# Kernel optimization log

Hardware: AMD Instinct MI355X
Metric: run time of the kernel (lower is better)

## Reference

```python
import jax, jax.numpy as jnp
import numpy as np

N_NODES = 100000

def setup_inputs() -> dict:
    key = jax.random.key(0)
    k1, k2, k3, k4 = jax.random.split(key, 4)
    feat = jax.random.normal(k1, (N_NODES, 128), dtype=jnp.float32)
    weight = jax.random.normal(k2, (128, 64), dtype=jnp.float32) * 0.05
    src = jax.random.randint(k3, (600000,), 0, N_NODES, dtype=jnp.int64)
    dst = jax.random.randint(k4, (600000,), 0, N_NODES, dtype=jnp.int64)
    return {"feat": feat, "weight": weight, "src": src, "dst": dst}

def reference(feat, weight, src, dst):
    n = feat.shape[0]
    ones = jnp.ones(src.shape[0], dtype=jnp.float32)
    # out-degree of source nodes (edges leave src), in-degree of dst nodes
    out_deg = jnp.clip(jax.ops.segment_sum(ones, src, num_segments=n), 1.0)
    in_deg = jnp.clip(jax.ops.segment_sum(ones, dst, num_segments=n), 1.0)
    norm_src = (out_deg ** -0.5)[:, None]   # [N,1]
    norm_dst = (in_deg ** -0.5)[:, None]    # [N,1]
    # in_feats (128) > out_feats (64): project first, then aggregate
    h = jnp.matmul(feat, weight) * norm_src              # [N, 64]
    msgs = h[src]                                        # [E, 64] gather
    rst = jax.ops.segment_sum(msgs, dst, num_segments=n)  # [N, 64] scatter-sum
    rst = rst * norm_dst
    return rst
```

## Files before the change

### kernel.cpp

```cpp
#include <hip/hip_runtime.h>
#include <hip/hip_fp16.h>

#define IN_F 128
#define OUT_F 64
#define NB    256
#define BSH   9
#define CAP   3840
#define CHUNK 2048
#define KPF  136
#define KPW  144

using short8  = __attribute__((ext_vector_type(8))) short;
using float4v = __attribute__((ext_vector_type(4))) float;

static __device__ inline unsigned short f2bf(float x) {
    union { float f; unsigned u; } v; v.f = x;
    unsigned r = (v.u + 0x7fffu + ((v.u >> 16) & 1u)) >> 16;
    return (unsigned short)r;
}

__global__ __launch_bounds__(256) void bin_gemm_kernel(
    const int* __restrict__ src, const int* __restrict__ dst,
    int* __restrict__ gcur_d, int* __restrict__ gcur_s,
    unsigned* __restrict__ bkt_d, unsigned short* __restrict__ bkt_s,
    int E, int nbin,
    const float* __restrict__ feat, const float* __restrict__ W,
    __half* __restrict__ h, int n)
{
    __shared__ union {
        struct { int hd[NB]; int hs[NB]; int based[NB]; int bases[NB]; } bin;
        struct { unsigned short Fh[128 * KPF]; unsigned short Wt[64 * KPW]; } gm;
    } smem;

    const int tid = threadIdx.x;

    if (blockIdx.x < (unsigned)nbin) {
        const int e0 = blockIdx.x * CHUNK;

        smem.bin.hd[tid] = 0; smem.bin.hs[tid] = 0;
        __syncthreads();

        int sv[8], dv[8];
        #pragma unroll
        for (int j = 0; j < 8; ++j) {
            int i = e0 + j * 256 + tid;
            if (i < E) { sv[j] = src[i]; dv[j] = dst[i]; }
            else       { sv[j] = -1;     dv[j] = -1; }
        }
        #pragma unroll
        for (int j = 0; j < 8; ++j) {
            if (dv[j] >= 0) {
                atomicAdd(&smem.bin.hd[dv[j] >> BSH], 1);
                atomicAdd(&smem.bin.hs[sv[j] >> BSH], 1);
            }
        }
        __syncthreads();

        int cd = smem.bin.hd[tid], cs = smem.bin.hs[tid];
        smem.bin.based[tid] = cd ? atomicAdd(&gcur_d[tid], cd) : 0;
        smem.bin.bases[tid] = cs ? atomicAdd(&gcur_s[tid], cs) : 0;
        smem.bin.hd[tid] = 0; smem.bin.hs[tid] = 0;
        __syncthreads();

        #pragma unroll
        for (int j = 0; j < 8; ++j) {
            if (dv[j] >= 0) {
                int bd = dv[j] >> BSH;
                int pd = atomicAdd(&smem.bin.hd[bd], 1) + smem.bin.based[bd];
                if (pd < CAP)
                    bkt_d[(size_t)bd * CAP + pd] =
                        (unsigned)sv[j] | ((unsigned)(dv[j] & 511) << 17);
                int bs = sv[j] >> BSH;
                int ps = atomicAdd(&smem.bin.hs[bs], 1) + smem.bin.bases[bs];
                if (ps < CAP) bkt_s[(size_t)bs * CAP + ps] = (unsigned short)(sv[j] & 511);
            }
        }
        return;
    }

    unsigned short* Fh = smem.gm.Fh;
    unsigned short* Wt = smem.gm.Wt;
    const int row0 = (blockIdx.x - nbin) * 128;

    {
        const float4* W4 = (const float4*)W;
        #pragma unroll
        for (int it = 0; it < 8; ++it) {
            int i4 = it * 256 + tid;
            int k  = i4 >> 4;
            int c4 = (i4 & 15) * 4;
            float4 wv = W4[i4];
            Wt[(c4 + 0) * KPW + k] = f2bf(wv.x);
            Wt[(c4 + 1) * KPW + k] = f2bf(wv.y);
            Wt[(c4 + 2) * KPW + k] = f2bf(wv.z);
            Wt[(c4 + 3) * KPW + k] = f2bf(wv.w);
        }
    }
    {
        const float4* F4 = (const float4*)feat;
        #pragma unroll
        for (int it = 0; it < 16; ++it) {
            int i4 = it * 256 + tid;
            int r  = i4 >> 5;
            int c4 = (i4 & 31) * 4;
            int gr = row0 + r; if (gr >= n) gr = n - 1;
            float4 v = F4[(long)gr * 32 + (i4 & 31)];
            ushort4 u;
            u.x = f2bf(v.x); u.y = f2bf(v.y); u.z = f2bf(v.z); u.w = f2bf(v.w);
            *(ushort4*)&Fh[r * KPF + c4] = u;
        }
    }
    __syncthreads();

    const int w  = tid >> 6;
    const int l  = tid & 63;
    const int ml = l & 15;
    const int q  = l >> 4;

    float4v acc[2][4];
    #pragma unroll
    for (int rt = 0; rt < 2; ++rt)
        #pragma unroll
        for (int ct = 0; ct < 4; ++ct)
            acc[rt][ct] = (float4v){0.f, 0.f, 0.f, 0.f};

    #pragma unroll
    for (int ks = 0; ks < 4; ++ks) {
        const int ko = ks * 32 + q * 8;
        short8 a0 = *(const short8*)&Fh[(w * 32 +  0 + ml) * KPF + ko];
        short8 a1 = *(const short8*)&Fh[(w * 32 + 16 + ml) * KPF + ko];
        short8 b0 = *(const short8*)&Wt[( 0 + ml) * KPW + ko];
        short8 b1 = *(const short8*)&Wt[(16 + ml) * KPW + ko];
        short8 b2 = *(const short8*)&Wt[(32 + ml) * KPW + ko];
        short8 b3 = *(const short8*)&Wt[(48 + ml) * KPW + ko];
        acc[0][0] = __builtin_amdgcn_mfma_f32_16x16x32_bf16(a0, b0, acc[0][0], 0, 0, 0);
        acc[0][1] = __builtin_amdgcn_mfma_f32_16x16x32_bf16(a0, b1, acc[0][1], 0, 0, 0);
        acc[0][2] = __builtin_amdgcn_mfma_f32_16x16x32_bf16(a0, b2, acc[0][2], 0, 0, 0);
        acc[0][3] = __builtin_amdgcn_mfma_f32_16x16x32_bf16(a0, b3, acc[0][3], 0, 0, 0);
        acc[1][0] = __builtin_amdgcn_mfma_f32_16x16x32_bf16(a1, b0, acc[1][0], 0, 0, 0);
        acc[1][1] = __builtin_amdgcn_mfma_f32_16x16x32_bf16(a1, b1, acc[1][1], 0, 0, 0);
        acc[1][2] = __builtin_amdgcn_mfma_f32_16x16x32_bf16(a1, b2, acc[1][2], 0, 0, 0);
        acc[1][3] = __builtin_amdgcn_mfma_f32_16x16x32_bf16(a1, b3, acc[1][3], 0, 0, 0);
    }

    #pragma unroll
    for (int rt = 0; rt < 2; ++rt) {
        #pragma unroll
        for (int reg = 0; reg < 4; ++reg) {
            int row = row0 + w * 32 + rt * 16 + q * 4 + reg;
            if (row < n) {
                #pragma unroll
                for (int ct = 0; ct < 4; ++ct)
                    h[(long)row * OUT_F + ct * 16 + ml] = __float2half(acc[rt][ct][reg]);
            }
        }
    }
}

__global__ __launch_bounds__(256) void csr_kernel(
    const unsigned* __restrict__ bkt_d, const unsigned short* __restrict__ bkt_s,
    const int* __restrict__ gcur_d, const int* __restrict__ gcur_s,
    int2* __restrict__ off_deg, int* __restrict__ ebuf, float* __restrict__ nsrc, int n)
{
    __shared__ int hist[512], curs[512], hist_s[512];
    __shared__ int wsum[4];
    const int b = blockIdx.x, tid = threadIdx.x;
    const int cnt   = min(gcur_d[b], CAP);
    const int cnt_s = min(gcur_s[b], CAP);

    hist[tid] = 0; hist[tid + 256] = 0;
    hist_s[tid] = 0; hist_s[tid + 256] = 0;
    __syncthreads();

    const unsigned* bp = bkt_d + (size_t)b * CAP;
    for (int i = tid; i < cnt; i += 256)
        atomicAdd(&hist[bp[i] >> 17], 1);
    for (int i = tid; i < cnt_s; i += 256)
        atomicAdd(&hist_s[bkt_s[(size_t)b * CAP + i]], 1);
    __syncthreads();

    int a0 = hist[2 * tid], a1 = hist[2 * tid + 1];
    int psum = a0 + a1;
    const int lane = tid & 63, w = tid >> 6;
    int x = psum;
    #pragma unroll
    for (int off = 1; off < 64; off <<= 1) {
        int y = __shfl_up(x, off);
        if (lane >= off) x += y;
    }
    if (lane == 63) wsum[w] = x;
    __syncthreads();
    int wbase = 0;
    for (int i = 0; i < w; ++i) wbase += wsum[i];
    int excl = x + wbase - psum;
    curs[2 * tid]     = excl;
    curs[2 * tid + 1] = excl + a0;
    off_deg[b * 512 + 2 * tid]     = make_int2(b * CAP + excl,      a0);
    off_deg[b * 512 + 2 * tid + 1] = make_int2(b * CAP + excl + a0, a1);
    __syncthreads();

    for (int i = tid; i < cnt; i += 256) {
        unsigned e = bp[i];
        int p = atomicAdd(&curs[e >> 17], 1);
        if (p < CAP) ebuf[b * CAP + p] = (int)(e & 0x1FFFFu);
    }

    int node = b * 512 + tid;
    if (node < n) nsrc[node] = rsqrtf(fmaxf((float)hist_s[tid], 1.0f));
    node += 256;
    if (node < n) nsrc[node] = rsqrtf(fmaxf((float)hist_s[tid + 256], 1.0f));
}

__global__ __launch_bounds__(256) void gather_kernel(
    const int* __restrict__ ebuf, const int2* __restrict__ off_deg,
    const float* __restrict__ nsrc,
    const __half* __restrict__ h, float* __restrict__ out, int n)
{
    int d = blockIdx.x * 4 + (threadIdx.x >> 6);
    int l = threadIdx.x & 63;
    int o = l >> 3;
    int t = l & 7;
    if (d >= n) return;
    int2 od = off_deg[d];
    int beg = od.x, m = od.y, end = od.x + od.y;
    float a0 = 0.f, a1 = 0.f, a2 = 0.f, a3 = 0.f;
    float a4 = 0.f, a5 = 0.f, a6 = 0.f, a7 = 0.f;
    for (int j = beg + o; j < end; j += 8) {
        int s = ebuf[j];
        float ns = nsrc[s];
        union { uint4 u; __half2 h2[4]; } P;
        P.u = *(const uint4*)&h[(long)s * OUT_F + 8 * t];
        float2 f0 = __half22float2(P.h2[0]);
        float2 f1 = __half22float2(P.h2[1]);
        float2 f2 = __half22float2(P.h2[2]);
        float2 f3 = __half22float2(P.h2[3]);
        a0 = fmaf(f0.x, ns, a0); a1 = fmaf(f0.y, ns, a1);
        a2 = fmaf(f1.x, ns, a2); a3 = fmaf(f1.y, ns, a3);
        a4 = fmaf(f2.x, ns, a4); a5 = fmaf(f2.y, ns, a5);
        a6 = fmaf(f3.x, ns, a6); a7 = fmaf(f3.y, ns, a7);
    }
    #pragma unroll
    for (int mask = 8; mask <= 32; mask <<= 1) {
        a0 += __shfl_xor(a0, mask); a1 += __shfl_xor(a1, mask);
        a2 += __shfl_xor(a2, mask); a3 += __shfl_xor(a3, mask);
        a4 += __shfl_xor(a4, mask); a5 += __shfl_xor(a5, mask);
        a6 += __shfl_xor(a6, mask); a7 += __shfl_xor(a7, mask);
    }
    if (o == 0) {
        float nd = rsqrtf(fmaxf((float)m, 1.0f));
        float4 v0 = make_float4(a0 * nd, a1 * nd, a2 * nd, a3 * nd);
        float4 v1 = make_float4(a4 * nd, a5 * nd, a6 * nd, a7 * nd);
        *(float4*)&out[(long)d * OUT_F + 8 * t]     = v0;
        *(float4*)&out[(long)d * OUT_F + 8 * t + 4] = v1;
    }
}

extern "C" void kernel_launch(void* const* d_in, const int* in_sizes, int n_in,
                              void* d_out, int out_size, void* d_ws, size_t ws_size,
                              hipStream_t stream) {
    const float* feat = (const float*)d_in[0];
    const float* W    = (const float*)d_in[1];
    const int*   src  = (const int*)d_in[2];
    const int*   dst  = (const int*)d_in[3];
    float* out = (float*)d_out;

    const int n = in_sizes[0] / IN_F;
    const int E = in_sizes[2];

    char* wsb = (char*)d_ws;
    int* gcur_d = (int*)wsb;
    int* gcur_s = gcur_d + NB;
    float* nsrc = (float*)(gcur_s + NB);
    size_t pos = (((size_t)(2 * NB + n)) * 4 + 15) & ~(size_t)15;
    int2* off_deg = (int2*)(wsb + pos);
    pos = (pos + (size_t)NB * 512 * 8 + 15) & ~(size_t)15;
    int* ebuf = (int*)(wsb + pos);
    pos = (pos + (size_t)NB * CAP * 4 + 15) & ~(size_t)15;
    unsigned* bkt_d = (unsigned*)(wsb + pos);
    pos = (pos + (size_t)NB * CAP * 4 + 15) & ~(size_t)15;
    unsigned short* bkt_s = (unsigned short*)(wsb + pos);
    pos = (pos + (size_t)NB * CAP * 2 + 15) & ~(size_t)15;
    __half* h = (__half*)(wsb + pos);

    hipMemsetAsync(gcur_d, 0, 2 * NB * sizeof(int), stream);

    const int nbin  = (E + CHUNK - 1) / CHUNK;
    const int ngemm = (n + 127) / 128;

    bin_gemm_kernel<<<nbin + ngemm, 256, 0, stream>>>(src, dst, gcur_d, gcur_s,
                                                      bkt_d, bkt_s, E, nbin,
                                                      feat, W, h, n);
    csr_kernel<<<NB, 256, 0, stream>>>(bkt_d, bkt_s, gcur_d, gcur_s,
                                       off_deg, ebuf, nsrc, n);
    gather_kernel<<<(n + 3) / 4, 256, 0, stream>>>(ebuf, off_deg, nsrc, h, out, n);
}
```

Before: 156.7 us.

## Fuse per-bin CSR sort into gather using shared-memory edge lists

Splits the CSR kernel into a small out-degree normalization kernel and a fused kernel that, per destination bin, counting-sorts edges into LDS and immediately performs the gather-aggregate for the bin's 512 nodes. This removes the global ebuf/off_deg round trip and one launch. In exchange, the gather now runs with only 256 blocks of 1024 threads, each holding about 15KB of LDS. That reduces parallelism and latency hiding for the random h gathers compared with the previous 25k-block gather launch.

```diff
diff --git a/kernel.cpp b/kernel.cpp
--- a/kernel.cpp
+++ b/kernel.cpp
@@ -157,101 +157,114 @@
     }
 }
 
-__global__ __launch_bounds__(256) void csr_kernel(
-    const unsigned* __restrict__ bkt_d, const unsigned short* __restrict__ bkt_s,
-    const int* __restrict__ gcur_d, const int* __restrict__ gcur_s,
-    int2* __restrict__ off_deg, int* __restrict__ ebuf, float* __restrict__ nsrc, int n)
+__global__ __launch_bounds__(256) void outdeg_kernel(
+    const unsigned short* __restrict__ bkt_s, const int* __restrict__ gcur_s,
+    float* __restrict__ nsrc, int n)
 {
-    __shared__ int hist[512], curs[512], hist_s[512];
-    __shared__ int wsum[4];
+    __shared__ int hs[512];
     const int b = blockIdx.x, tid = threadIdx.x;
-    const int cnt   = min(gcur_d[b], CAP);
     const int cnt_s = min(gcur_s[b], CAP);
 
-    hist[tid] = 0; hist[tid + 256] = 0;
-    hist_s[tid] = 0; hist_s[tid + 256] = 0;
-    __syncthreads();
-
+    hs[tid] = 0; hs[tid + 256] = 0;
+    __syncthreads();
+
+    const unsigned short* bp = bkt_s + (size_t)b * CAP;
+    for (int i = tid; i < cnt_s; i += 256)
+        atomicAdd(&hs[bp[i]], 1);
+    __syncthreads();
+
+    int node = b * 512 + tid;
+    if (node < n) nsrc[node] = rsqrtf(fmaxf((float)hs[tid], 1.0f));
+    node += 256;
+    if (node < n) nsrc[node] = rsqrtf(fmaxf((float)hs[tid + 256], 1.0f));
+}
+
+__global__ __launch_bounds__(1024) void sortgather_kernel(
+    const unsigned* __restrict__ bkt_d, const int* __restrict__ gcur_d,
+    const float* __restrict__ nsrc,
+    const __half* __restrict__ h, float* __restrict__ out, int n)
+{
+    __shared__ int sstart[512];
+    __shared__ int sdeg[512];
+    __shared__ int curs[512];
+    __shared__ int wsum[8];
+    __shared__ int elist[CAP];
+
+    const int b = blockIdx.x, tid = threadIdx.x;
+    const int cnt = min(gcur_d[b], CAP);
     const unsigned* bp = bkt_d + (size_t)b * CAP;
-    for (int i = tid; i < cnt; i += 256)
-        atomicAdd(&hist[bp[i] >> 17], 1);
-    for (int i = tid; i < cnt_s; i += 256)
-        atomicAdd(&hist_s[bkt_s[(size_t)b * CAP + i]], 1);
-    __syncthreads();
-
-    int a0 = hist[2 * tid], a1 = hist[2 * tid + 1];
-    int psum = a0 + a1;
-    const int lane = tid & 63, w = tid >> 6;
-    int x = psum;
+
+    if (tid < 512) sdeg[tid] = 0;
+    __syncthreads();
+
+    for (int i = tid; i < cnt; i += 1024)
+        atomicAdd(&sdeg[bp[i] >> 17], 1);
+    __syncthreads();
+
+    const int lane = tid & 63;
+    int deg = (tid < 512) ? sdeg[tid] : 0;
+    int x = deg;
     #pragma unroll
     for (int off = 1; off < 64; off <<= 1) {
         int y = __shfl_up(x, off);
         if (lane >= off) x += y;
     }
-    if (lane == 63) wsum[w] = x;
-    __syncthreads();
-    int wbase = 0;
-    for (int i = 0; i < w; ++i) wbase += wsum[i];
-    int excl = x + wbase - psum;
-    curs[2 * tid]     = excl;
-    curs[2 * tid + 1] = excl + a0;
-    off_deg[b * 512 + 2 * tid]     = make_int2(b * CAP + excl,      a0);
-    off_deg[b * 512 + 2 * tid + 1] = make_int2(b * CAP + excl + a0, a1);
-    __syncthreads();
-
-    for (int i = tid; i < cnt; i += 256) {
+    if (tid < 512 && lane == 63) wsum[tid >> 6] = x;
+    __syncthreads();
+    if (tid < 512) {
+        int wv = tid >> 6, wbase = 0;
+        for (int i = 0; i < wv; ++i) wbase += wsum[i];
+        int excl = x + wbase - deg;
+        sstart[tid] = excl;
+        curs[tid]   = excl;
+    }
+    __syncthreads();
+
+    for (int i = tid; i < cnt; i += 1024) {
         unsigned e = bp[i];
         int p = atomicAdd(&curs[e >> 17], 1);
-        if (p < CAP) ebuf[b * CAP + p] = (int)(e & 0x1FFFFu);
-    }
-
-    int node = b * 512 + tid;
-    if (node < n) nsrc[node] = rsqrtf(fmaxf((float)hist_s[tid], 1.0f));
-    node += 256;
-    if (node < n) nsrc[node] = rsqrtf(fmaxf((float)hist_s[tid + 256], 1.0f));
-}
-
-__global__ __launch_bounds__(256) void gather_kernel(
-    const int* __restrict__ ebuf, const int2* __restrict__ off_deg,
-    const float* __restrict__ nsrc,
-    const __half* __restrict__ h, float* __restrict__ out, int n)
-{
-    int d = blockIdx.x * 4 + (threadIdx.x >> 6);
-    int l = threadIdx.x & 63;
-    int o = l >> 3;
-    int t = l & 7;
-    if (d >= n) return;
-    int2 od = off_deg[d];
-    int beg = od.x, m = od.y, end = od.x + od.y;
-    float a0 = 0.f, a1 = 0.f, a2 = 0.f, a3 = 0.f;
-    float a4 = 0.f, a5 = 0.f, a6 = 0.f, a7 = 0.f;
-    for (int j = beg + o; j < end; j += 8) {
-        int s = ebuf[j];
-        float ns = nsrc[s];
-        union { uint4 u; __half2 h2[4]; } P;
-        P.u = *(const uint4*)&h[(long)s * OUT_F + 8 * t];
-        float2 f0 = __half22float2(P.h2[0]);
-        float2 f1 = __half22float2(P.h2[1]);
-        float2 f2 = __half22float2(P.h2[2]);
-        float2 f3 = __half22float2(P.h2[3]);
-        a0 = fmaf(f0.x, ns, a0); a1 = fmaf(f0.y, ns, a1);
-        a2 = fmaf(f1.x, ns, a2); a3 = fmaf(f1.y, ns, a3);
-        a4 = fmaf(f2.x, ns, a4); a5 = fmaf(f2.y, ns, a5);
-        a6 = fmaf(f3.x, ns, a6); a7 = fmaf(f3.y, ns, a7);
-    }
-    #pragma unroll
-    for (int mask = 8; mask <= 32; mask <<= 1) {
-        a0 += __shfl_xor(a0, mask); a1 += __shfl_xor(a1, mask);
-        a2 += __shfl_xor(a2, mask); a3 += __shfl_xor(a3, mask);
-        a4 += __shfl_xor(a4, mask); a5 += __shfl_xor(a5, mask);
-        a6 += __shfl_xor(a6, mask); a7 += __shfl_xor(a7, mask);
-    }
-    if (o == 0) {
-        float nd = rsqrtf(fmaxf((float)m, 1.0f));
-        float4 v0 = make_float4(a0 * nd, a1 * nd, a2 * nd, a3 * nd);
-        float4 v1 = make_float4(a4 * nd, a5 * nd, a6 * nd, a7 * nd);
-        *(float4*)&out[(long)d * OUT_F + 8 * t]     = v0;
-        *(float4*)&out[(long)d * OUT_F + 8 * t + 4] = v1;
+        if (p < CAP) elist[p] = (int)(e & 0x1FFFFu);
+    }
+    __syncthreads();
+
+    const int wv = tid >> 6;
+    const int o  = lane >> 3;
+    const int t  = lane & 7;
+    for (int dl = wv; dl < 512; dl += 16) {
+        int node = b * 512 + dl;
+        if (node >= n) break;
+        int beg = sstart[dl], m = sdeg[dl], end = beg + m;
+        float a0 = 0.f, a1 = 0.f, a2 = 0.f, a3 = 0.f;
+        float a4 = 0.f, a5 = 0.f, a6 = 0.f, a7 = 0.f;
+        for (int j = beg + o; j < end; j += 8) {
+            int s = elist[j];
+            float ns = nsrc[s];
+            union { uint4 u; __half2 h2[4]; } P;
+            P.u = *(const uint4*)&h[(long)s * OUT_F + 8 * t];
+            float2 f0 = __half22float2(P.h2[0]);
+            float2 f1 = __half22float2(P.h2[1]);
+            float2 f2 = __half22float2(P.h2[2]);
+            float2 f3 = __half22float2(P.h2[3]);
+            a0 = fmaf(f0.x, ns, a0); a1 = fmaf(f0.y, ns, a1);
+            a2 = fmaf(f1.x, ns, a2); a3 = fmaf(f1.y, ns, a3);
+            a4 = fmaf(f2.x, ns, a4); a5 = fmaf(f2.y, ns, a5);
+            a6 = fmaf(f3.x, ns, a6); a7 = fmaf(f3.y, ns, a7);
+        }
+        #pragma unroll
+        for (int mask = 8; mask <= 32; mask <<= 1) {
+            a0 += __shfl_xor(a0, mask); a1 += __shfl_xor(a1, mask);
+            a2 += __shfl_xor(a2, mask); a3 += __shfl_xor(a3, mask);
+            a4 += __shfl_xor(a4, mask); a5 += __shfl_xor(a5, mask);
+            a6 += __shfl_xor(a6, mask); a7 += __shfl_xor(a7, mask);
+        }
+        if (o == 0) {
+            float nd = rsqrtf(fmaxf((float)m, 1.0f));
+            float4 v0 = make_float4(a0 * nd, a1 * nd, a2 * nd, a3 * nd);
+            float4 v1 = make_float4(a4 * nd, a5 * nd, a6 * nd, a7 * nd);
+            float* op = &out[(long)node * OUT_F + 8 * t];
+            *(float4*)op       = v0;
+            *(float4*)(op + 4) = v1;
+        }
     }
 }
 
@@ -272,10 +285,6 @@
     int* gcur_s = gcur_d + NB;
     float* nsrc = (float*)(gcur_s + NB);
     size_t pos = (((size_t)(2 * NB + n)) * 4 + 15) & ~(size_t)15;
-    int2* off_deg = (int2*)(wsb + pos);
-    pos = (pos + (size_t)NB * 512 * 8 + 15) & ~(size_t)15;
-    int* ebuf = (int*)(wsb + pos);
-    pos = (pos + (size_t)NB * CAP * 4 + 15) & ~(size_t)15;
     unsigned* bkt_d = (unsigned*)(wsb + pos);
     pos = (pos + (size_t)NB * CAP * 4 + 15) & ~(size_t)15;
     unsigned short* bkt_s = (unsigned short*)(wsb + pos);
@@ -290,7 +299,6 @@
     bin_gemm_kernel<<<nbin + ngemm, 256, 0, stream>>>(src, dst, gcur_d, gcur_s,
                                                       bkt_d, bkt_s, E, nbin,
                                                       feat, W, h, n);
-    csr_kernel<<<NB, 256, 0, stream>>>(bkt_d, bkt_s, gcur_d, gcur_s,
-                                       off_deg, ebuf, nsrc, n);
-    gather_kernel<<<(n + 3) / 4, 256, 0, stream>>>(ebuf, off_deg, nsrc, h, out, n);
-}
+    outdeg_kernel<<<NB, 256, 0, stream>>>(bkt_s, gcur_s, nsrc, n);
+    sortgather_kernel<<<NB, 1024, 0, stream>>>(bkt_d, gcur_d, nsrc, h, out, n);
+}
```

Result: slower. 166.0 us (+5.9%).

## Map one destination node per 8-lane group in gather, drop cross-lane reduction

Applied to the files above, without the earlier changes.

The gather kernel now gives each 8-lane group its own destination node, so a wavefront handles 8 nodes instead of one. Each group walks its own edge list serially, two edges per iteration for more memory-level parallelism. This removes the xor-shuffle reduction and the idle lanes on short edge lists. The grid shrinks to n/32 blocks. In exchange, load imbalance between groups with different degrees causes divergence within a wavefront.

```diff
diff --git a/kernel.cpp b/kernel.cpp
--- a/kernel.cpp
+++ b/kernel.cpp
@@ -216,16 +216,46 @@
     const float* __restrict__ nsrc,
     const __half* __restrict__ h, float* __restrict__ out, int n)
 {
-    int d = blockIdx.x * 4 + (threadIdx.x >> 6);
-    int l = threadIdx.x & 63;
-    int o = l >> 3;
-    int t = l & 7;
+    const int lane = threadIdx.x & 63;
+    const int wv   = threadIdx.x >> 6;
+    const int o    = lane >> 3;
+    const int t    = lane & 7;
+    const int d    = blockIdx.x * 32 + wv * 8 + o;
     if (d >= n) return;
+
     int2 od = off_deg[d];
-    int beg = od.x, m = od.y, end = od.x + od.y;
+    const int beg = od.x, m = od.y, end = beg + m;
+
     float a0 = 0.f, a1 = 0.f, a2 = 0.f, a3 = 0.f;
     float a4 = 0.f, a5 = 0.f, a6 = 0.f, a7 = 0.f;
-    for (int j = beg + o; j < end; j += 8) {
+
+    int j = beg;
+    for (; j + 1 < end; j += 2) {
+        int sA = ebuf[j];
+        int sB = ebuf[j + 1];
+        float nsA = nsrc[sA];
+        float nsB = nsrc[sB];
+        union { uint4 u; __half2 h2[4]; } PA, PB;
+        PA.u = *(const uint4*)&h[(long)sA * OUT_F + 8 * t];
+        PB.u = *(const uint4*)&h[(long)sB * OUT_F + 8 * t];
+        float2 fA0 = __half22float2(PA.h2[0]);
+        float2 fA1 = __half22float2(PA.h2[1]);
+        float2 fA2 = __half22float2(PA.h2[2]);
+        float2 fA3 = __half22float2(PA.h2[3]);
+        a0 = fmaf(fA0.x, nsA, a0); a1 = fmaf(fA0.y, nsA, a1);
+        a2 = fmaf(fA1.x, nsA, a2); a3 = fmaf(fA1.y, nsA, a3);
+        a4 = fmaf(fA2.x, nsA, a4); a5 = fmaf(fA2.y, nsA, a5);
+        a6 = fmaf(fA3.x, nsA, a6); a7 = fmaf(fA3.y, nsA, a7);
+        float2 fB0 = __half22float2(PB.h2[0]);
+        float2 fB1 = __half22float2(PB.h2[1]);
+        float2 fB2 = __half22float2(PB.h2[2]);
+        float2 fB3 = __half22float2(PB.h2[3]);
+        a0 = fmaf(fB0.x, nsB, a0); a1 = fmaf(fB0.y, nsB, a1);
+        a2 = fmaf(fB1.x, nsB, a2); a3 = fmaf(fB1.y, nsB, a3);
+        a4 = fmaf(fB2.x, nsB, a4); a5 = fmaf(fB2.y, nsB, a5);
+        a6 = fmaf(fB3.x, nsB, a6); a7 = fmaf(fB3.y, nsB, a7);
+    }
+    if (j < end) {
         int s = ebuf[j];
         float ns = nsrc[s];
         union { uint4 u; __half2 h2[4]; } P;
@@ -239,20 +269,13 @@
         a4 = fmaf(f2.x, ns, a4); a5 = fmaf(f2.y, ns, a5);
         a6 = fmaf(f3.x, ns, a6); a7 = fmaf(f3.y, ns, a7);
     }
-    #pragma unroll
-    for (int mask = 8; mask <= 32; mask <<= 1) {
-        a0 += __shfl_xor(a0, mask); a1 += __shfl_xor(a1, mask);
-        a2 += __shfl_xor(a2, mask); a3 += __shfl_xor(a3, mask);
-        a4 += __shfl_xor(a4, mask); a5 += __shfl_xor(a5, mask);
-        a6 += __shfl_xor(a6, mask); a7 += __shfl_xor(a7, mask);
-    }
-    if (o == 0) {
-        float nd = rsqrtf(fmaxf((float)m, 1.0f));
-        float4 v0 = make_float4(a0 * nd, a1 * nd, a2 * nd, a3 * nd);
-        float4 v1 = make_float4(a4 * nd, a5 * nd, a6 * nd, a7 * nd);
-        *(float4*)&out[(long)d * OUT_F + 8 * t]     = v0;
-        *(float4*)&out[(long)d * OUT_F + 8 * t + 4] = v1;
-    }
+
+    float nd = rsqrtf(fmaxf((float)m, 1.0f));
+    float4 v0 = make_float4(a0 * nd, a1 * nd, a2 * nd, a3 * nd);
+    float4 v1 = make_float4(a4 * nd, a5 * nd, a6 * nd, a7 * nd);
+    float* op = &out[(long)d * OUT_F + 8 * t];
+    *(float4*)op       = v0;
+    *(float4*)(op + 4) = v1;
 }
 
 extern "C" void kernel_launch(void* const* d_in, const int* in_sizes, int n_in,
@@ -292,5 +315,5 @@
                                                       feat, W, h, n);
     csr_kernel<<<NB, 256, 0, stream>>>(bkt_d, bkt_s, gcur_d, gcur_s,
                                        off_deg, ebuf, nsrc, n);
-    gather_kernel<<<(n + 3) / 4, 256, 0, stream>>>(ebuf, off_deg, nsrc, h, out, n);
-}
+    gather_kernel<<<(n + 31) / 32, 256, 0, stream>>>(ebuf, off_deg, nsrc, h, out, n);
+}
```

Result: faster. 145.3 us (-7.3%).

## Interleave bin and GEMM blocks; gather two nodes per 8-lane group

Applied to the files above, without the earlier changes.

The fused bin/GEMM launch now spreads binning blocks evenly across the grid instead of running them all first, so the atomic-heavy binning overlaps with GEMM work. The gather kernel is reorganized: each group of 8 lanes owns two destination nodes and walks their edge lists serially with 2-way unrolling and two independent accumulator sets. This removes the cross-lane shuffle reduction and the lanes idled by low-degree nodes, and gives more loads in flight per lane. In exchange, per-node work is serial, so high-degree nodes lengthen the critical path, and lanes within a wave diverge on differing degrees.

```diff
diff --git a/kernel.cpp b/kernel.cpp
--- a/kernel.cpp
+++ b/kernel.cpp
@@ -33,9 +33,14 @@
     } smem;
 
     const int tid = threadIdx.x;
-
-    if (blockIdx.x < (unsigned)nbin) {
-        const int e0 = blockIdx.x * CHUNK;
+    const int b   = blockIdx.x;
+    const int G   = gridDim.x;
+    const int f   = (int)(((long)b       * nbin) / G);
+    const int c   = (int)(((long)(b + 1) * nbin) / G);
+    const bool is_bin = (c > f);
+
+    if (is_bin) {
+        const int e0 = f * CHUNK;
 
         smem.bin.hd[tid] = 0; smem.bin.hs[tid] = 0;
         __syncthreads();
@@ -80,7 +85,7 @@
 
     unsigned short* Fh = smem.gm.Fh;
     unsigned short* Wt = smem.gm.Wt;
-    const int row0 = (blockIdx.x - nbin) * 128;
+    const int row0 = (b - f) * 128;
 
     {
         const float4* W4 = (const float4*)W;
@@ -211,47 +216,82 @@
     if (node < n) nsrc[node] = rsqrtf(fmaxf((float)hist_s[tid + 256], 1.0f));
 }
 
+static __device__ inline void acc_edge(
+    const int* __restrict__ ebuf, const float* __restrict__ nsrc,
+    const __half* __restrict__ h, int j, int t,
+    float& a0, float& a1, float& a2, float& a3,
+    float& a4, float& a5, float& a6, float& a7)
+{
+    int s = ebuf[j];
+    float ns = nsrc[s];
+    union { uint4 u; __half2 h2[4]; } P;
+    P.u = *(const uint4*)&h[(long)s * OUT_F + 8 * t];
+    float2 f0 = __half22float2(P.h2[0]);
+    float2 f1 = __half22float2(P.h2[1]);
+    float2 f2 = __half22float2(P.h2[2]);
+    float2 f3 = __half22float2(P.h2[3]);
+    a0 = fmaf(f0.x, ns, a0); a1 = fmaf(f0.y, ns, a1);
+    a2 = fmaf(f1.x, ns, a2); a3 = fmaf(f1.y, ns, a3);
+    a4 = fmaf(f2.x, ns, a4); a5 = fmaf(f2.y, ns, a5);
+    a6 = fmaf(f3.x, ns, a6); a7 = fmaf(f3.y, ns, a7);
+}
+
 __global__ __launch_bounds__(256) void gather_kernel(
     const int* __restrict__ ebuf, const int2* __restrict__ off_deg,
     const float* __restrict__ nsrc,
     const __half* __restrict__ h, float* __restrict__ out, int n)
 {
-    int d = blockIdx.x * 4 + (threadIdx.x >> 6);
-    int l = threadIdx.x & 63;
-    int o = l >> 3;
-    int t = l & 7;
-    if (d >= n) return;
-    int2 od = off_deg[d];
-    int beg = od.x, m = od.y, end = od.x + od.y;
+    const int s_idx = threadIdx.x >> 3;
+    const int t     = threadIdx.x & 7;
+    const int d0    = blockIdx.x * 64 + s_idx;
+    const int d1    = d0 + 32;
+    if (d0 >= n) return;
+
+    int2 odA = off_deg[d0];
+    int2 odB = (d1 < n) ? off_deg[d1] : make_int2(0, 0);
+    int jA = odA.x, endA = odA.x + odA.y;
+    int jB = odB.x, endB = odB.x + odB.y;
+
     float a0 = 0.f, a1 = 0.f, a2 = 0.f, a3 = 0.f;
     float a4 = 0.f, a5 = 0.f, a6 = 0.f, a7 = 0.f;
-    for (int j = beg + o; j < end; j += 8) {
-        int s = ebuf[j];
-        float ns = nsrc[s];
-        union { uint4 u; __half2 h2[4]; } P;
-        P.u = *(const uint4*)&h[(long)s * OUT_F + 8 * t];
-        float2 f0 = __half22float2(P.h2[0]);
-        float2 f1 = __half22float2(P.h2[1]);
-        float2 f2 = __half22float2(P.h2[2]);
-        float2 f3 = __half22float2(P.h2[3]);
-        a0 = fmaf(f0.x, ns, a0); a1 = fmaf(f0.y, ns, a1);
-        a2 = fmaf(f1.x, ns, a2); a3 = fmaf(f1.y, ns, a3);
-        a4 = fmaf(f2.x, ns, a4); a5 = fmaf(f2.y, ns, a5);
-        a6 = fmaf(f3.x, ns, a6); a7 = fmaf(f3.y, ns, a7);
-    }
-    #pragma unroll
-    for (int mask = 8; mask <= 32; mask <<= 1) {
-        a0 += __shfl_xor(a0, mask); a1 += __shfl_xor(a1, mask);
-        a2 += __shfl_xor(a2, mask); a3 += __shfl_xor(a3, mask);
-        a4 += __shfl_xor(a4, mask); a5 += __shfl_xor(a5, mask);
-        a6 += __shfl_xor(a6, mask); a7 += __shfl_xor(a7, mask);
-    }
-    if (o == 0) {
-        float nd = rsqrtf(fmaxf((float)m, 1.0f));
+    float b0 = 0.f, b1 = 0.f, b2 = 0.f, b3 = 0.f;
+    float b4 = 0.f, b5 = 0.f, b6 = 0.f, b7 = 0.f;
+
+    while (jA + 1 < endA && jB + 1 < endB) {
+        acc_edge(ebuf, nsrc, h, jA,     t, a0,a1,a2,a3,a4,a5,a6,a7);
+        acc_edge(ebuf, nsrc, h, jA + 1, t, a0,a1,a2,a3,a4,a5,a6,a7);
+        acc_edge(ebuf, nsrc, h, jB,     t, b0,b1,b2,b3,b4,b5,b6,b7);
+        acc_edge(ebuf, nsrc, h, jB + 1, t, b0,b1,b2,b3,b4,b5,b6,b7);
+        jA += 2; jB += 2;
+    }
+    while (jA + 1 < endA) {
+        acc_edge(ebuf, nsrc, h, jA,     t, a0,a1,a2,a3,a4,a5,a6,a7);
+        acc_edge(ebuf, nsrc, h, jA + 1, t, a0,a1,a2,a3,a4,a5,a6,a7);
+        jA += 2;
+    }
+    while (jB + 1 < endB) {
+        acc_edge(ebuf, nsrc, h, jB,     t, b0,b1,b2,b3,b4,b5,b6,b7);
+        acc_edge(ebuf, nsrc, h, jB + 1, t, b0,b1,b2,b3,b4,b5,b6,b7);
+        jB += 2;
+    }
+    if (jA < endA) acc_edge(ebuf, nsrc, h, jA, t, a0,a1,a2,a3,a4,a5,a6,a7);
+    if (jB < endB) acc_edge(ebuf, nsrc, h, jB, t, b0,b1,b2,b3,b4,b5,b6,b7);
+
+    {
+        float nd = rsqrtf(fmaxf((float)odA.y, 1.0f));
         float4 v0 = make_float4(a0 * nd, a1 * nd, a2 * nd, a3 * nd);
         float4 v1 = make_float4(a4 * nd, a5 * nd, a6 * nd, a7 * nd);
-        *(float4*)&out[(long)d * OUT_F + 8 * t]     = v0;
-        *(float4*)&out[(long)d * OUT_F + 8 * t + 4] = v1;
+        float* op = &out[(long)d0 * OUT_F + 8 * t];
+        *(float4*)op       = v0;
+        *(float4*)(op + 4) = v1;
+    }
+    if (d1 < n) {
+        float nd = rsqrtf(fmaxf((float)odB.y, 1.0f));
+        float4 v0 = make_float4(b0 * nd, b1 * nd, b2 * nd, b3 * nd);
+        float4 v1 = make_float4(b4 * nd, b5 * nd, b6 * nd, b7 * nd);
+        float* op = &out[(long)d1 * OUT_F + 8 * t];
+        *(float4*)op       = v0;
+        *(float4*)(op + 4) = v1;
     }
 }
 
@@ -292,5 +332,5 @@
                                                       feat, W, h, n);
     csr_kernel<<<NB, 256, 0, stream>>>(bkt_d, bkt_s, gcur_d, gcur_s,
                                        off_deg, ebuf, nsrc, n);
-    gather_kernel<<<(n + 3) / 4, 256, 0, stream>>>(ebuf, off_deg, nsrc, h, out, n);
-}
+    gather_kernel<<<(n + 63) / 64, 256, 0, stream>>>(ebuf, off_deg, nsrc, h, out, n);
+}
```

After: 144.0 us. 8.1% less time.
